# Kernel tuning notes

Hardware: AMD Instinct MI355X
Metric: run time of the kernel (lower is better)

Reference implementation:

```python
import jax, jax.numpy as jnp
import numpy as np

DIM = 512
HEADS = 8
DIM_HEAD = 64
SCALE = DIM_HEAD ** -0.5


def setup_inputs() -> dict:
    key = jax.random.key(0)
    k1, k2, k3, k4, k5 = jax.random.split(key, 5)
    inner = HEADS * DIM_HEAD
    x = jax.random.normal(k1, (16, DIM, 32, 32), dtype=jnp.float32)
    W_proj = jax.random.normal(k2, (DIM, inner * 3), dtype=jnp.float32) * (DIM ** -0.5)
    b_proj = jax.random.normal(k3, (inner * 3,), dtype=jnp.float32) * 0.01
    W_out = jax.random.normal(k4, (inner, DIM), dtype=jnp.float32) * (inner ** -0.5)
    b_out = jax.random.normal(k5, (DIM,), dtype=jnp.float32) * 0.01
    return {"x": x, "W_proj": W_proj, "b_proj": b_proj, "W_out": W_out, "b_out": b_out}


def reference(x, W_proj, b_proj, W_out, b_out):
    b, c, hh, ww = x.shape
    s = hh * ww
    xs = x.reshape(b, c, s).transpose(0, 2, 1)  # b s c
    qkv = xs @ W_proj + b_proj                  # b s (heads * 3*dim_head)
    qkv = qkv.reshape(b, s, HEADS, 3 * DIM_HEAD)
    q, k, v = jnp.split(qkv, 3, axis=-1)        # each: b s h d
    w = jnp.einsum('bshd,bthd->bsth', q, k) * SCALE
    w = jax.nn.softmax(w, axis=2)
    res = jnp.einsum('bsth,bthd->bshd', w, v).reshape(b, s, HEADS * DIM_HEAD)
    out = res @ W_out + b_out + xs              # b s c (residual)
    return out.transpose(0, 2, 1).reshape(b, c, hh, ww)
```

## Files before the change

kernel.cpp:

```cpp
#include <hip/hip_runtime.h>
#include <hip/hip_bf16.h>

#define BATCH 16
#define CDIM  512
#define SEQ   1024
#define HEADS 8
#define DHEAD 64
#define N3    1536
#define QSCALE 0.18033688011112042f

typedef unsigned short ushort_t;
typedef __attribute__((ext_vector_type(8))) short short8;
typedef __attribute__((ext_vector_type(4))) float f32x4;

__device__ __forceinline__ unsigned f2bf(float f) {
    unsigned u = __float_as_uint(f);
    u += 0x7fffu + ((u >> 16) & 1u);
    return u >> 16;
}
__device__ __forceinline__ float fast_exp2(float x) {
    float r;
    asm("v_exp_f32 %0, %1" : "=v"(r) : "v"(x));
    return r;
}
__device__ __forceinline__ unsigned pack_bf16_trunc(float lo, float hi) {
    return __builtin_amdgcn_perm(__float_as_uint(hi), __float_as_uint(lo), 0x07060302u);
}
__device__ __forceinline__ void async16(const void* g, void* l) {
    __builtin_amdgcn_global_load_lds(
        (const __attribute__((address_space(1))) unsigned int*)g,
        (__attribute__((address_space(3))) unsigned int*)l, 16, 0, 0);
}
__device__ __forceinline__ void barrier_raw() {
    __builtin_amdgcn_sched_barrier(0);
    __builtin_amdgcn_s_barrier();
    __builtin_amdgcn_sched_barrier(0);
}
#define WAIT_VMCNT(n) asm volatile("s_waitcnt vmcnt(" #n ")" ::: "memory")


__global__ __launch_bounds__(256) void blockify_kernel(
    const float* __restrict__ in, ushort_t* __restrict__ out, int C)
{
    __shared__ float t[64][65];
    const int k0 = blockIdx.y * 64, c0 = blockIdx.x * 64;
    const float* inb = in + (size_t)blockIdx.z * 512 * C;
    const int tid = threadIdx.x;
#pragma unroll
    for (int i = 0; i < 16; ++i) {
        int idx = tid + i * 256;
        int r = idx >> 6, c = idx & 63;
        t[r][c] = inb[(size_t)(k0 + r) * C + c0 + c];
    }
    __syncthreads();
    const size_t mbase = (size_t)blockIdx.z * C + c0;
    const int ml = tid & 63;
#pragma unroll
    for (int i = 0; i < 2; ++i) {
        int oct = (tid >> 6) + i * 4;
        size_t m = mbase + ml;
        int mt = (int)(m >> 7), mr = (int)(m & 127);
        int m16 = mr >> 4, col = mr & 15;
        int k = k0 + oct * 8;
        int it = k >> 5, q = (k >> 3) & 3;
        uint4 pk;
        pk.x = f2bf(t[oct * 8 + 0][ml]) | (f2bf(t[oct * 8 + 1][ml]) << 16);
        pk.y = f2bf(t[oct * 8 + 2][ml]) | (f2bf(t[oct * 8 + 3][ml]) << 16);
        pk.z = f2bf(t[oct * 8 + 4][ml]) | (f2bf(t[oct * 8 + 5][ml]) << 16);
        pk.w = f2bf(t[oct * 8 + 6][ml]) | (f2bf(t[oct * 8 + 7][ml]) << 16);
        size_t off = ((size_t)(mt * 16 + it) * 8 + m16) * 512 + (q * 16 + col) * 8;
        *(uint4*)&out[off] = pk;
    }
}

__global__ __launch_bounds__(256) void qkv_gemm_kernel(
    const ushort_t* __restrict__ xtb, const ushort_t* __restrict__ WpTb,
    const float* __restrict__ bp,
    ushort_t* __restrict__ q_buf, ushort_t* __restrict__ kb,
    ushort_t* __restrict__ vb)
{
    __shared__ alignas(16) ushort_t Asub[2][8 * 512];
    __shared__ alignas(16) ushort_t Bsub[2][8 * 512];

    const int tid = threadIdx.x, w = tid >> 6, lane = tid & 63;
    const int quad = lane >> 4, col = lane & 15;
    const int wm = w >> 1, wn = w & 1;

    const int lin = blockIdx.x + 12 * blockIdx.y;
    const int xcd = lin & 7;
    const int rr  = lin >> 3;
    const int n0  = (rr % 12) * 128;
    const int m0  = ((rr / 12) * 8 + xcd) * 128;

    f32x4 acc[4][4];
#pragma unroll
    for (int i = 0; i < 4; ++i)
#pragma unroll
        for (int j = 0; j < 4; ++j) acc[i][j] = (f32x4){0.f, 0.f, 0.f, 0.f};

    const ushort_t* Ab = xtb  + (size_t)(m0 >> 7) * 65536 + (w * 2) * 512 + lane * 8;
    const ushort_t* Bb = WpTb + (size_t)(n0 >> 7) * 65536 + (w * 2) * 512 + lane * 8;

#define QKV_STAGE(buf, t)                                         \
    do {                                                          \
        async16(Ab + (t) * 4096,       &Asub[buf][(w * 2 + 0) * 512]); \
        async16(Ab + (t) * 4096 + 512, &Asub[buf][(w * 2 + 1) * 512]); \
        async16(Bb + (t) * 4096,       &Bsub[buf][(w * 2 + 0) * 512]); \
        async16(Bb + (t) * 4096 + 512, &Bsub[buf][(w * 2 + 1) * 512]); \
    } while (0)

    QKV_STAGE(0, 0);
    QKV_STAGE(1, 1);
    for (int it = 0; it < 16; ++it) {
        const int cur = it & 1;
        if (it < 15) { WAIT_VMCNT(4); } else { WAIT_VMCNT(0); }
        barrier_raw();

        short8 af[4], bfr[4];
#pragma unroll
        for (int i = 0; i < 4; ++i) af[i]  = *(const short8*)&Asub[cur][(wm * 4 + i) * 512 + lane * 8];
#pragma unroll
        for (int j = 0; j < 4; ++j) bfr[j] = *(const short8*)&Bsub[cur][(wn * 4 + j) * 512 + lane * 8];
#pragma unroll
        for (int i = 0; i < 4; ++i)
#pragma unroll
            for (int j = 0; j < 4; ++j)
                acc[i][j] = __builtin_amdgcn_mfma_f32_16x16x32_bf16(af[i], bfr[j], acc[i][j], 0, 0, 0);

        if (it < 14) {
            barrier_raw();
            QKV_STAGE(cur, it + 2);
        }
    }
#undef QKV_STAGE

    const int b = m0 >> 10, s0 = m0 & 1023;
    const size_t b8 = (size_t)b * HEADS;
#pragma unroll
    for (int j = 0; j < 4; ++j) {
        int nb = n0 + wn * 64 + j * 16;
        int h = nb / 192, rem = nb % 192;
        int type = rem >> 6, dbase = rem & 63;
        float bias = bp[nb + col];
        size_t bh = b8 + h;
        int d = dbase + col;
#pragma unroll
        for (int i = 0; i < 4; ++i) {
            int sb = s0 + wm * 64 + i * 16 + quad * 4;
            f32x4 v = acc[i][j];
            if (type == 2) {
                unsigned lo = f2bf(v[0] + bias) | (f2bf(v[1] + bias) << 16);
                unsigned hi = f2bf(v[2] + bias) | (f2bf(v[3] + bias) << 16);
                uint2 pk; pk.x = lo; pk.y = hi;
                int itv = sb >> 6, sub = (d >> 4) * 2 + ((sb >> 5) & 1);
                size_t off = ((bh * 16 + itv) * 8 + sub) * 512
                           + (((sb >> 2) & 3) * 16 + (d & 15)) * 8
                           + ((sb >> 4) & 1) * 4;
                *(uint2*)&vb[off] = pk;
            } else if (type == 1) {
#pragma unroll
                for (int r = 0; r < 4; ++r) {
                    int t = sb + r;
                    int itk = t >> 6, sub = ((t >> 4) & 3) * 2 + (d >> 5);
                    size_t off = ((bh * 16 + itk) * 8 + sub) * 512
                               + (((d >> 3) & 3) * 16 + (t & 15)) * 8 + (d & 7);
                    kb[off] = (ushort_t)f2bf(v[r] + bias);
                }
            } else {
#pragma unroll
                for (int r = 0; r < 4; ++r)
                    q_buf[(bh * SEQ + sb + r) * DHEAD + d] =
                        (ushort_t)f2bf((v[r] + bias) * QSCALE);
            }
        }
    }
}

__global__ __launch_bounds__(128) void attn_kernel(
    const ushort_t* __restrict__ q_buf, const ushort_t* __restrict__ kb,
    const ushort_t* __restrict__ vb, ushort_t* __restrict__ resb)
{
    __shared__ alignas(16) ushort_t Kf[2][8 * 512];
    __shared__ alignas(16) ushort_t Vf[2][8 * 512];

    const int tid  = threadIdx.x;
    const int w    = tid >> 6;
    const int lane = tid & 63;
    const int quad = lane >> 4;
    const int col  = lane & 15;

    const int bhid = blockIdx.x;
    const int b = bhid >> 3, h = bhid & 7;
    const int q0 = blockIdx.y * 128;
    const size_t bh = (size_t)b * HEADS + h;

    const ushort_t* qp = q_buf + ((bh * SEQ) + q0 + w * 64 + col) * DHEAD + quad * 8;
    short8 qf0[4], qf1[4];
#pragma unroll
    for (int g = 0; g < 4; ++g) {
        qf0[g] = *(const short8*)(qp + g * 16 * DHEAD);
        qf1[g] = *(const short8*)(qp + g * 16 * DHEAD + 32);
    }

    short8 ones;
#pragma unroll
    for (int i = 0; i < 8; ++i) ones[i] = (short)0x3F80;

    f32x4 O[4][4];
#pragma unroll
    for (int g = 0; g < 4; ++g)
#pragma unroll
        for (int i = 0; i < 4; ++i) O[g][i] = (f32x4){0.f, 0.f, 0.f, 0.f};
    f32x4 L[4];
#pragma unroll
    for (int g = 0; g < 4; ++g) L[g] = (f32x4){0.f, 0.f, 0.f, 0.f};

    const ushort_t* kaB = kb + (size_t)bh * 65536 + (w * 4) * 512 + lane * 8;
    const ushort_t* vaB = vb + (size_t)bh * 65536 + (w * 4) * 512 + lane * 8;

#define ATTN_STAGE(buf)                                            \
    do {                                                           \
        async16(kaB,        &Kf[buf][(w * 4 + 0) * 512]);          \
        async16(kaB + 512,  &Kf[buf][(w * 4 + 1) * 512]);          \
        async16(kaB + 1024, &Kf[buf][(w * 4 + 2) * 512]);          \
        async16(kaB + 1536, &Kf[buf][(w * 4 + 3) * 512]);          \
        async16(vaB,        &Vf[buf][(w * 4 + 0) * 512]);          \
        async16(vaB + 512,  &Vf[buf][(w * 4 + 1) * 512]);          \
        async16(vaB + 1024, &Vf[buf][(w * 4 + 2) * 512]);          \
        async16(vaB + 1536, &Vf[buf][(w * 4 + 3) * 512]);          \
        kaB += 4096;                                               \
        vaB += 4096;                                               \
    } while (0)

    ATTN_STAGE(0);

    for (int it = 0; it < 16; ++it) {
        const int cur = it & 1;
        const ushort_t* kc = Kf[cur];
        const ushort_t* vc = Vf[cur];
        __syncthreads();
        if (it < 15) ATTN_STAGE(cur ^ 1);

        short8 kf[8];
#pragma unroll
        for (int t16 = 0; t16 < 4; ++t16) {
            kf[2 * t16 + 0] = *(const short8*)&kc[(t16 * 2 + 0) * 512 + lane * 8];
            kf[2 * t16 + 1] = *(const short8*)&kc[(t16 * 2 + 1) * 512 + lane * 8];
        }

        short8 pf[4][2];
#pragma unroll
        for (int g = 0; g < 4; ++g) {
            f32x4 S[4];
            __builtin_amdgcn_s_setprio(1);
#pragma unroll
            for (int t16 = 0; t16 < 4; ++t16) {
                f32x4 a = (f32x4){0.f, 0.f, 0.f, 0.f};
                a = __builtin_amdgcn_mfma_f32_16x16x32_bf16(kf[2 * t16 + 0], qf0[g], a, 0, 0, 0);
                a = __builtin_amdgcn_mfma_f32_16x16x32_bf16(kf[2 * t16 + 1], qf1[g], a, 0, 0, 0);
                S[t16] = a;
            }
            __builtin_amdgcn_s_setprio(0);
            union { uint4 u; short8 s; } p0, p1;
            p0.u.x = pack_bf16_trunc(fast_exp2(S[0][0]), fast_exp2(S[0][1]));
            p0.u.y = pack_bf16_trunc(fast_exp2(S[0][2]), fast_exp2(S[0][3]));
            p0.u.z = pack_bf16_trunc(fast_exp2(S[1][0]), fast_exp2(S[1][1]));
            p0.u.w = pack_bf16_trunc(fast_exp2(S[1][2]), fast_exp2(S[1][3]));
            p1.u.x = pack_bf16_trunc(fast_exp2(S[2][0]), fast_exp2(S[2][1]));
            p1.u.y = pack_bf16_trunc(fast_exp2(S[2][2]), fast_exp2(S[2][3]));
            p1.u.z = pack_bf16_trunc(fast_exp2(S[3][0]), fast_exp2(S[3][1]));
            p1.u.w = pack_bf16_trunc(fast_exp2(S[3][2]), fast_exp2(S[3][3]));
            pf[g][0] = p0.s;
            pf[g][1] = p1.s;
        }

#pragma unroll
        for (int d16 = 0; d16 < 4; ++d16) {
            const short8 v0 = *(const short8*)&vc[(d16 * 2 + 0) * 512 + lane * 8];
            const short8 v1 = *(const short8*)&vc[(d16 * 2 + 1) * 512 + lane * 8];
            __builtin_amdgcn_s_setprio(1);
#pragma unroll
            for (int g = 0; g < 4; ++g) {
                O[g][d16] = __builtin_amdgcn_mfma_f32_16x16x32_bf16(pf[g][0], v0, O[g][d16], 0, 0, 0);
                O[g][d16] = __builtin_amdgcn_mfma_f32_16x16x32_bf16(pf[g][1], v1, O[g][d16], 0, 0, 0);
            }
            __builtin_amdgcn_s_setprio(0);
        }
#pragma unroll
        for (int g = 0; g < 4; ++g) {
            L[g] = __builtin_amdgcn_mfma_f32_16x16x32_bf16(pf[g][0], ones, L[g], 0, 0, 0);
            L[g] = __builtin_amdgcn_mfma_f32_16x16x32_bf16(pf[g][1], ones, L[g], 0, 0, 0);
        }
    }
#undef ATTN_STAGE

    const int mt = b * 8 + (q0 >> 7);
#pragma unroll
    for (int g = 0; g < 4; ++g) {
        const int m16 = w * 4 + g;
#pragma unroll
        for (int r = 0; r < 4; ++r) {
            float inv = 1.f / L[g][r];
            const int mcol = quad * 4 + r;
#pragma unroll
            for (int d16 = 0; d16 < 4; ++d16) {
                int itk = h * 2 + (d16 >> 1);
                int kq = (d16 & 1) * 2 + (col >> 3);
                size_t off = ((size_t)(mt * 16 + itk) * 8 + m16) * 512
                           + (kq * 16 + mcol) * 8 + (col & 7);
                resb[off] = (ushort_t)f2bf(O[g][d16][r] * inv);
            }
        }
    }
}

__global__ __launch_bounds__(256) void out_gemm_kernel(
    const ushort_t* __restrict__ resb, const ushort_t* __restrict__ WoTb,
    const float* __restrict__ bo, const float* __restrict__ x,
    float* __restrict__ out)
{
    __shared__ alignas(16) ushort_t Asub[2][8 * 512];
    __shared__ alignas(16) ushort_t Bsub[2][8 * 512];

    const int tid = threadIdx.x, w = tid >> 6, lane = tid & 63;
    const int quad = lane >> 4, col = lane & 15;
    const int wm = w >> 1, wn = w & 1;

    const int lin = blockIdx.x + 4 * blockIdx.y;
    const int xcd = lin & 7;
    const int rr  = lin >> 3;
    const int n0  = (rr & 3) * 128;
    const int m0  = ((rr >> 2) * 8 + xcd) * 128;

    f32x4 acc[4][4];
#pragma unroll
    for (int i = 0; i < 4; ++i)
#pragma unroll
        for (int j = 0; j < 4; ++j) acc[i][j] = (f32x4){0.f, 0.f, 0.f, 0.f};

    const ushort_t* Ab = resb + (size_t)(m0 >> 7) * 65536 + (w * 2) * 512 + lane * 8;
    const ushort_t* Bb = WoTb + (size_t)(n0 >> 7) * 65536 + (w * 2) * 512 + lane * 8;

#define OUT_STAGE(buf, t)                                         \
    do {                                                          \
        async16(Ab + (t) * 4096,       &Asub[buf][(w * 2 + 0) * 512]); \
        async16(Ab + (t) * 4096 + 512, &Asub[buf][(w * 2 + 1) * 512]); \
        async16(Bb + (t) * 4096,       &Bsub[buf][(w * 2 + 0) * 512]); \
        async16(Bb + (t) * 4096 + 512, &Bsub[buf][(w * 2 + 1) * 512]); \
    } while (0)

    OUT_STAGE(0, 0);
    OUT_STAGE(1, 1);
    for (int it = 0; it < 16; ++it) {
        const int cur = it & 1;
        if (it < 15) { WAIT_VMCNT(4); } else { WAIT_VMCNT(0); }
        barrier_raw();

        short8 af[4], bfr[4];
#pragma unroll
        for (int i = 0; i < 4; ++i) af[i]  = *(const short8*)&Asub[cur][(wm * 4 + i) * 512 + lane * 8];
#pragma unroll
        for (int j = 0; j < 4; ++j) bfr[j] = *(const short8*)&Bsub[cur][(wn * 4 + j) * 512 + lane * 8];
#pragma unroll
        for (int i = 0; i < 4; ++i)
#pragma unroll
            for (int j = 0; j < 4; ++j)
                acc[i][j] = __builtin_amdgcn_mfma_f32_16x16x32_bf16(af[i], bfr[j], acc[i][j], 0, 0, 0);

        if (it < 14) {
            barrier_raw();
            OUT_STAGE(cur, it + 2);
        }
    }
#undef OUT_STAGE

    const int b = m0 >> 10, s0 = m0 & 1023;
#pragma unroll
    for (int j = 0; j < 4; ++j) {
        int n = n0 + wn * 64 + j * 16 + col;
        float bias = bo[n];
#pragma unroll
        for (int i = 0; i < 4; ++i) {
            int sb = s0 + wm * 64 + i * 16 + quad * 4;
            size_t o = ((size_t)b * CDIM + n) * SEQ + sb;
            float4 xr = *(const float4*)&x[o];
            f32x4 v = acc[i][j];
            float4 ov;
            ov.x = v[0] + bias + xr.x;
            ov.y = v[1] + bias + xr.y;
            ov.z = v[2] + bias + xr.z;
            ov.w = v[3] + bias + xr.w;
            *(float4*)&out[o] = ov;
        }
    }
}

extern "C" void kernel_launch(void* const* d_in, const int* in_sizes, int n_in,
                              void* d_out, int out_size, void* d_ws, size_t ws_size,
                              hipStream_t stream) {
    const float* x  = (const float*)d_in[0];
    const float* Wp = (const float*)d_in[1];
    const float* bp = (const float*)d_in[2];
    const float* Wo = (const float*)d_in[3];
    const float* bo = (const float*)d_in[4];
    float* out = (float*)d_out;

    ushort_t* xtb   = (ushort_t*)d_ws;
    ushort_t* WpTb  = xtb   + (size_t)8388608;
    ushort_t* WoTb  = WpTb  + (size_t)786432;
    ushort_t* q_buf = WoTb  + (size_t)262144;
    ushort_t* kb    = q_buf + (size_t)8388608;
    ushort_t* vb    = kb    + (size_t)8388608;
    ushort_t* resb  = vb    + (size_t)8388608;

    blockify_kernel<<<dim3(16, 8, 16), 256, 0, stream>>>(x,  xtb,  1024);
    blockify_kernel<<<dim3(24, 8, 1),  256, 0, stream>>>(Wp, WpTb, 1536);
    blockify_kernel<<<dim3(8, 8, 1),   256, 0, stream>>>(Wo, WoTb, 512);
    qkv_gemm_kernel<<<dim3(12, 128), 256, 0, stream>>>(xtb, WpTb, bp, q_buf, kb, vb);
    attn_kernel<<<dim3(128, 8), 128, 0, stream>>>(q_buf, kb, vb, resb);
    out_gemm_kernel<<<dim3(4, 128), 256, 0, stream>>>(resb, WoTb, bo, x, out);
}
```

Measured before the change: 196.0 us.

## Software-pipeline QK and PV groups in attention loop to overlap exp with MFMA

Restructures the attention inner loop so the QK^T scores for the next query group are computed while the current group's exp/pack and PV/rowsum MFMAs are issued. The two groups interleave through double-buffered S registers. V fragments are now preloaded into registers up front, and the s_setprio hints are removed. The aim is to hide transcendental and VALU latency behind matrix-core work, at the cost of more live VGPRs, which could lower occupancy or cause spills.

```diff
diff --git a/kernel.cpp b/kernel.cpp
--- a/kernel.cpp
+++ b/kernel.cpp
@@ -232,6 +232,38 @@
         vaB += 4096;                                               \
     } while (0)
 
+#define QK_GRP(Sdst, g)                                                       \
+    do {                                                                      \
+        _Pragma("unroll")                                                     \
+        for (int t16 = 0; t16 < 4; ++t16) {                                   \
+            f32x4 a = (f32x4){0.f, 0.f, 0.f, 0.f};                            \
+            a = __builtin_amdgcn_mfma_f32_16x16x32_bf16(kf[2 * t16 + 0], qf0[g], a, 0, 0, 0); \
+            a = __builtin_amdgcn_mfma_f32_16x16x32_bf16(kf[2 * t16 + 1], qf1[g], a, 0, 0, 0); \
+            Sdst[t16] = a;                                                    \
+        }                                                                     \
+    } while (0)
+
+#define CONSUME_GRP(g, S)                                                     \
+    do {                                                                      \
+        union { uint4 u; short8 s; } p0_, p1_;                                \
+        p0_.u.x = pack_bf16_trunc(fast_exp2(S[0][0]), fast_exp2(S[0][1]));    \
+        p0_.u.y = pack_bf16_trunc(fast_exp2(S[0][2]), fast_exp2(S[0][3]));    \
+        p0_.u.z = pack_bf16_trunc(fast_exp2(S[1][0]), fast_exp2(S[1][1]));    \
+        p0_.u.w = pack_bf16_trunc(fast_exp2(S[1][2]), fast_exp2(S[1][3]));    \
+        p1_.u.x = pack_bf16_trunc(fast_exp2(S[2][0]), fast_exp2(S[2][1]));    \
+        p1_.u.y = pack_bf16_trunc(fast_exp2(S[2][2]), fast_exp2(S[2][3]));    \
+        p1_.u.z = pack_bf16_trunc(fast_exp2(S[3][0]), fast_exp2(S[3][1]));    \
+        p1_.u.w = pack_bf16_trunc(fast_exp2(S[3][2]), fast_exp2(S[3][3]));    \
+        const short8 pf0_ = p0_.s, pf1_ = p1_.s;                              \
+        _Pragma("unroll")                                                     \
+        for (int d16 = 0; d16 < 4; ++d16) {                                   \
+            O[g][d16] = __builtin_amdgcn_mfma_f32_16x16x32_bf16(pf0_, vf[2 * d16 + 0], O[g][d16], 0, 0, 0); \
+            O[g][d16] = __builtin_amdgcn_mfma_f32_16x16x32_bf16(pf1_, vf[2 * d16 + 1], O[g][d16], 0, 0, 0); \
+        }                                                                     \
+        L[g] = __builtin_amdgcn_mfma_f32_16x16x32_bf16(pf0_, ones, L[g], 0, 0, 0); \
+        L[g] = __builtin_amdgcn_mfma_f32_16x16x32_bf16(pf1_, ones, L[g], 0, 0, 0); \
+    } while (0)
+
     ATTN_STAGE(0);
 
     for (int it = 0; it < 16; ++it) {
@@ -241,58 +273,31 @@
         __syncthreads();
         if (it < 15) ATTN_STAGE(cur ^ 1);
 
-        short8 kf[8];
+        short8 kf[8], vf[8];
 #pragma unroll
         for (int t16 = 0; t16 < 4; ++t16) {
             kf[2 * t16 + 0] = *(const short8*)&kc[(t16 * 2 + 0) * 512 + lane * 8];
             kf[2 * t16 + 1] = *(const short8*)&kc[(t16 * 2 + 1) * 512 + lane * 8];
         }
-
-        short8 pf[4][2];
-#pragma unroll
-        for (int g = 0; g < 4; ++g) {
-            f32x4 S[4];
-            __builtin_amdgcn_s_setprio(1);
-#pragma unroll
-            for (int t16 = 0; t16 < 4; ++t16) {
-                f32x4 a = (f32x4){0.f, 0.f, 0.f, 0.f};
-                a = __builtin_amdgcn_mfma_f32_16x16x32_bf16(kf[2 * t16 + 0], qf0[g], a, 0, 0, 0);
-                a = __builtin_amdgcn_mfma_f32_16x16x32_bf16(kf[2 * t16 + 1], qf1[g], a, 0, 0, 0);
-                S[t16] = a;
-            }
-            __builtin_amdgcn_s_setprio(0);
-            union { uint4 u; short8 s; } p0, p1;
-            p0.u.x = pack_bf16_trunc(fast_exp2(S[0][0]), fast_exp2(S[0][1]));
-            p0.u.y = pack_bf16_trunc(fast_exp2(S[0][2]), fast_exp2(S[0][3]));
-            p0.u.z = pack_bf16_trunc(fast_exp2(S[1][0]), fast_exp2(S[1][1]));
-            p0.u.w = pack_bf16_trunc(fast_exp2(S[1][2]), fast_exp2(S[1][3]));
-            p1.u.x = pack_bf16_trunc(fast_exp2(S[2][0]), fast_exp2(S[2][1]));
-            p1.u.y = pack_bf16_trunc(fast_exp2(S[2][2]), fast_exp2(S[2][3]));
-            p1.u.z = pack_bf16_trunc(fast_exp2(S[3][0]), fast_exp2(S[3][1]));
-            p1.u.w = pack_bf16_trunc(fast_exp2(S[3][2]), fast_exp2(S[3][3]));
-            pf[g][0] = p0.s;
-            pf[g][1] = p1.s;
-        }
-
 #pragma unroll
         for (int d16 = 0; d16 < 4; ++d16) {
-            const short8 v0 = *(const short8*)&vc[(d16 * 2 + 0) * 512 + lane * 8];
-            const short8 v1 = *(const short8*)&vc[(d16 * 2 + 1) * 512 + lane * 8];
-            __builtin_amdgcn_s_setprio(1);
-#pragma unroll
-            for (int g = 0; g < 4; ++g) {
-                O[g][d16] = __builtin_amdgcn_mfma_f32_16x16x32_bf16(pf[g][0], v0, O[g][d16], 0, 0, 0);
-                O[g][d16] = __builtin_amdgcn_mfma_f32_16x16x32_bf16(pf[g][1], v1, O[g][d16], 0, 0, 0);
-            }
-            __builtin_amdgcn_s_setprio(0);
-        }
-#pragma unroll
-        for (int g = 0; g < 4; ++g) {
-            L[g] = __builtin_amdgcn_mfma_f32_16x16x32_bf16(pf[g][0], ones, L[g], 0, 0, 0);
-            L[g] = __builtin_amdgcn_mfma_f32_16x16x32_bf16(pf[g][1], ones, L[g], 0, 0, 0);
-        }
+            vf[2 * d16 + 0] = *(const short8*)&vc[(d16 * 2 + 0) * 512 + lane * 8];
+            vf[2 * d16 + 1] = *(const short8*)&vc[(d16 * 2 + 1) * 512 + lane * 8];
+        }
+
+        f32x4 Sa[4], Sb[4];
+        QK_GRP(Sa, 0);
+        QK_GRP(Sb, 1);
+        CONSUME_GRP(0, Sa);
+        QK_GRP(Sa, 2);
+        CONSUME_GRP(1, Sb);
+        QK_GRP(Sb, 3);
+        CONSUME_GRP(2, Sa);
+        CONSUME_GRP(3, Sb);
     }
 #undef ATTN_STAGE
+#undef QK_GRP
+#undef CONSUME_GRP
 
     const int mt = b * 8 + (q0 >> 7);
 #pragma unroll
```

Measured after the change: 204.6 us. 1.04x slower.
